# Optimization experiments

Hardware: AMD Instinct MI355X
Metric: run time of the kernel (lower is better)

Reference implementation:

```python
import jax, jax.numpy as jnp
import numpy as np

BN_EPS = 1e-5


def setup_inputs() -> dict:
    key = jax.random.key(0)
    k1, k2, k3 = jax.random.split(key, 3)
    C = 192
    inputs = jax.random.normal(k1, (32, C, 112, 112), dtype=jnp.float32)
    # Depthwise kernels: one 3x3 filter per channel -> OIHW with I=1, groups=C
    w = jax.random.normal(k2, (C, 1, 3, 3), dtype=jnp.float32) * 0.1
    b = jax.random.normal(k3, (C,), dtype=jnp.float32) * 0.1
    gamma = jnp.ones((C,), dtype=jnp.float32)
    beta = jnp.zeros((C,), dtype=jnp.float32)
    return {"inputs": inputs, "w": w, "b": b, "gamma": gamma, "beta": beta}


def reference(inputs, w, b, gamma, beta):
    C = w.shape[0]
    stride = 1
    # Depthwise 3x3 conv (equivalent to the per-channel Conv2d loop + concat)
    y = jax.lax.conv_general_dilated(
        inputs, w,
        window_strides=(stride, stride),
        padding=((1, 1), (1, 1)),
        dimension_numbers=("NCHW", "OIHW", "NCHW"),
        feature_group_count=C,
    ) + b[None, :, None, None]
    # BatchNorm2d in training mode: batch statistics over (N, H, W), biased var
    mean = jnp.mean(y, axis=(0, 2, 3), keepdims=True)
    var = jnp.mean(jnp.square(y - mean), axis=(0, 2, 3), keepdims=True)
    y_hat = (y - mean) * jax.lax.rsqrt(var + BN_EPS)
    z = gamma[None, :, None, None] * y_hat + beta[None, :, None, None]
    # ReLU6
    return jnp.clip(z, 0.0, 6.0)
```

## Files before the change

kernel.cpp:

```cpp
#include <hip/hip_runtime.h>

#define C_   192
#define N_   32
#define H_   112
#define W_   112
#define W4   28
#define V_   4
#define HT   (H_ / V_)
#define P2   (HT * W4)
#define BLK  256
#define GX   ((P2 + BLK - 1) / BLK)

__global__ void zero_acc_kernel(float* __restrict__ acc) {
    for (int i = threadIdx.x; i < 2 * C_; i += blockDim.x) acc[i] = 0.0f;
}

struct Row { float l; float4 m; float r; };

__device__ __forceinline__ Row load_row(const float* __restrict__ row, int j) {
    const float* p = row + 4 * j;
    Row r;
    r.m = *(const float4*)p;
    r.l = (j > 0)      ? p[-1] : 0.0f;
    r.r = (j < W4 - 1) ? p[4]  : 0.0f;
    return r;
}

__device__ __forceinline__ void fma_row(const Row& r, float w0, float w1, float w2,
                                        float4& a) {
    a.x += w0 * r.l   + w1 * r.m.x + w2 * r.m.y;
    a.y += w0 * r.m.x + w1 * r.m.y + w2 * r.m.z;
    a.z += w0 * r.m.y + w1 * r.m.z + w2 * r.m.w;
    a.w += w0 * r.m.z + w1 * r.m.w + w2 * r.r;
}

__device__ __forceinline__ void conv_tile(const float* __restrict__ plane,
                                          int ht, int j, const float* wc,
                                          float4 y[V_]) {
    Row rows[V_ + 2];
    const float* rp = plane + (size_t)(ht * V_) * W_;
    if (ht > 0) rows[0] = load_row(rp - W_, j);
    else        rows[0] = Row{0.f, {0.f, 0.f, 0.f, 0.f}, 0.f};
#pragma unroll
    for (int v = 0; v < V_; ++v) rows[1 + v] = load_row(rp + v * W_, j);
    if (ht < HT - 1) rows[V_ + 1] = load_row(rp + (size_t)V_ * W_, j);
    else             rows[V_ + 1] = Row{0.f, {0.f, 0.f, 0.f, 0.f}, 0.f};

#pragma unroll
    for (int v = 0; v < V_; ++v) {
        float4 a = {0.f, 0.f, 0.f, 0.f};
        fma_row(rows[v],     wc[0], wc[1], wc[2], a);
        fma_row(rows[v + 1], wc[3], wc[4], wc[5], a);
        fma_row(rows[v + 2], wc[6], wc[7], wc[8], a);
        y[v] = a;
    }
}

__global__ __launch_bounds__(BLK) void stats_kernel(const float* __restrict__ in,
                                                    const float* __restrict__ w,
                                                    float* __restrict__ acc) {
    const int nc = blockIdx.y;
    const int c  = nc % C_;
    const int t  = blockIdx.x * BLK + threadIdx.x;

    float wc[9];
#pragma unroll
    for (int k = 0; k < 9; ++k) wc[k] = w[c * 9 + k];

    float s = 0.0f, ss = 0.0f;
    if (t < P2) {
        const int ht = t / W4, j = t % W4;
        const float* plane = in + (size_t)nc * (H_ * W_);
        float4 y[V_];
        conv_tile(plane, ht, j, wc, y);
#pragma unroll
        for (int v = 0; v < V_; ++v) {
            s  += (y[v].x + y[v].y) + (y[v].z + y[v].w);
            ss += (y[v].x * y[v].x + y[v].y * y[v].y)
                + (y[v].z * y[v].z + y[v].w * y[v].w);
        }
    }

#pragma unroll
    for (int off = 32; off > 0; off >>= 1) {
        s  += __shfl_down(s,  off, 64);
        ss += __shfl_down(ss, off, 64);
    }
    __shared__ float ls[BLK / 64], lss[BLK / 64];
    const int lane = threadIdx.x & 63;
    const int wv   = threadIdx.x >> 6;
    if (lane == 0) { ls[wv] = s; lss[wv] = ss; }
    __syncthreads();
    if (threadIdx.x == 0) {
        float S  = 0.f, SS = 0.f;
#pragma unroll
        for (int i = 0; i < BLK / 64; ++i) { S += ls[i]; SS += lss[i]; }
        atomicAdd(&acc[c],      S);
        atomicAdd(&acc[C_ + c], SS);
    }
}

__global__ void finalize_kernel(const float* __restrict__ acc,
                                const float* __restrict__ gamma,
                                const float* __restrict__ beta,
                                float* __restrict__ st) {
    const int c = threadIdx.x;
    if (c < C_) {
        const float M    = (float)N_ * (float)H_ * (float)W_;
        const float mean = acc[c] / M;
        float var        = acc[C_ + c] / M - mean * mean;
        var              = fmaxf(var, 0.0f);
        const float sc   = gamma[c] * rsqrtf(var + 1e-5f);
        st[c]       = sc;
        st[C_ + c]  = beta[c] - sc * mean;
    }
}

__global__ __launch_bounds__(BLK) void apply_kernel(const float* __restrict__ in,
                                                    const float* __restrict__ w,
                                                    const float* __restrict__ st,
                                                    float* __restrict__ out) {
    const int nc = blockIdx.y;
    const int c  = nc % C_;
    const int t  = blockIdx.x * BLK + threadIdx.x;
    if (t >= P2) return;

    float wc[9];
#pragma unroll
    for (int k = 0; k < 9; ++k) wc[k] = w[c * 9 + k];
    const float sc = st[c];
    const float sh = st[C_ + c];

    const int ht = t / W4, j = t % W4;
    const float* plane = in + (size_t)nc * (H_ * W_);
    float4 y[V_];
    conv_tile(plane, ht, j, wc, y);

    float* orow = out + (size_t)nc * (H_ * W_) + (size_t)(ht * V_) * W_ + 4 * j;
#pragma unroll
    for (int v = 0; v < V_; ++v) {
        float4 z;
        z.x = fminf(fmaxf(sc * y[v].x + sh, 0.0f), 6.0f);
        z.y = fminf(fmaxf(sc * y[v].y + sh, 0.0f), 6.0f);
        z.z = fminf(fmaxf(sc * y[v].z + sh, 0.0f), 6.0f);
        z.w = fminf(fmaxf(sc * y[v].w + sh, 0.0f), 6.0f);
        *(float4*)(orow + (size_t)v * W_) = z;
    }
}

extern "C" void kernel_launch(void* const* d_in, const int* in_sizes, int n_in,
                              void* d_out, int out_size, void* d_ws, size_t ws_size,
                              hipStream_t stream) {
    const float* in    = (const float*)d_in[0];
    const float* w     = (const float*)d_in[1];
    const float* gamma = (const float*)d_in[3];
    const float* beta  = (const float*)d_in[4];
    float* out = (float*)d_out;

    float* acc = (float*)d_ws;
    float* st  = acc + 2 * C_;

    hipLaunchKernelGGL(zero_acc_kernel, dim3(1), dim3(64), 0, stream, acc);

    const dim3 grid(GX, N_ * C_);
    hipLaunchKernelGGL(stats_kernel, grid, dim3(BLK), 0, stream, in, w, acc);
    hipLaunchKernelGGL(finalize_kernel, dim3(1), dim3(C_), 0, stream,
                       acc, gamma, beta, st);
    hipLaunchKernelGGL(apply_kernel, grid, dim3(BLK), 0, stream, in, w, st, out);
}
```

Before: 617.2 us.

## Remap threads to 32-lane row tiles with shuffle halos and reversed apply order

Threads are regrouped so each 32-lane half-wave covers one 4-row strip of a plane (28 active lanes), and the grid becomes 1D over all strips. Left and right halo values now come from cross-lane shuffles instead of extra scalar global loads. The stats reduction now does one atomic pair per half-wave, with no shared-memory stage. The apply kernel walks blocks in reverse order so it starts on data the stats pass touched last and is more likely still cached, and it writes output with nontemporal stores. The cost is 4 idle lanes per 32, and many more atomics on the same per-channel accumulators.

```diff
diff --git a/kernel.cpp b/kernel.cpp
--- a/kernel.cpp
+++ b/kernel.cpp
@@ -4,12 +4,15 @@
 #define N_   32
 #define H_   112
 #define W_   112
-#define W4   28
 #define V_   4
 #define HT   (H_ / V_)
-#define P2   (HT * W4)
+#define NC   (N_ * C_)
+#define NRT  (NC * HT)
 #define BLK  256
-#define GX   ((P2 + BLK - 1) / BLK)
+#define HWPB (BLK / 32)
+#define NBLK (NRT / HWPB)
+
+typedef float vf4 __attribute__((ext_vector_type(4)));
 
 __global__ void zero_acc_kernel(float* __restrict__ acc) {
     for (int i = threadIdx.x; i < 2 * C_; i += blockDim.x) acc[i] = 0.0f;
@@ -17,12 +20,14 @@
 
 struct Row { float l; float4 m; float r; };
 
-__device__ __forceinline__ Row load_row(const float* __restrict__ row, int j) {
-    const float* p = row + 4 * j;
+__device__ __forceinline__ Row load_row_sh(const float* __restrict__ p,
+                                           bool has_l, bool has_r) {
     Row r;
     r.m = *(const float4*)p;
-    r.l = (j > 0)      ? p[-1] : 0.0f;
-    r.r = (j < W4 - 1) ? p[4]  : 0.0f;
+    const float lv = __shfl_up(r.m.w, 1, 64);
+    const float rv = __shfl_down(r.m.x, 1, 64);
+    r.l = has_l ? lv : 0.0f;
+    r.r = has_r ? rv : 0.0f;
     return r;
 }
 
@@ -35,17 +40,25 @@
 }
 
 __device__ __forceinline__ void conv_tile(const float* __restrict__ plane,
-                                          int ht, int j, const float* wc,
-                                          float4 y[V_]) {
+                                          int ht, int jeff, bool hl, bool hr,
+                                          const float* wc, float4 y[V_]) {
+    const float* rp = plane + (size_t)(ht * V_) * W_ + 4 * jeff;
     Row rows[V_ + 2];
-    const float* rp = plane + (size_t)(ht * V_) * W_;
-    if (ht > 0) rows[0] = load_row(rp - W_, j);
-    else        rows[0] = Row{0.f, {0.f, 0.f, 0.f, 0.f}, 0.f};
+    {
+        const float* p = (ht > 0) ? (rp - W_) : rp;
+        Row r = load_row_sh(p, hl, hr);
+        if (ht == 0) { r.l = 0.f; r.m = make_float4(0.f, 0.f, 0.f, 0.f); r.r = 0.f; }
+        rows[0] = r;
+    }
 #pragma unroll
-    for (int v = 0; v < V_; ++v) rows[1 + v] = load_row(rp + v * W_, j);
-    if (ht < HT - 1) rows[V_ + 1] = load_row(rp + (size_t)V_ * W_, j);
-    else             rows[V_ + 1] = Row{0.f, {0.f, 0.f, 0.f, 0.f}, 0.f};
-
+    for (int v = 0; v < V_; ++v)
+        rows[1 + v] = load_row_sh(rp + v * W_, hl, hr);
+    {
+        const float* p = (ht < HT - 1) ? (rp + V_ * W_) : rp;
+        Row r = load_row_sh(p, hl, hr);
+        if (ht == HT - 1) { r.l = 0.f; r.m = make_float4(0.f, 0.f, 0.f, 0.f); r.r = 0.f; }
+        rows[V_ + 1] = r;
+    }
 #pragma unroll
     for (int v = 0; v < V_; ++v) {
         float4 a = {0.f, 0.f, 0.f, 0.f};
@@ -56,23 +69,28 @@
     }
 }
 
-__global__ __launch_bounds__(BLK) void stats_kernel(const float* __restrict__ in,
-                                                    const float* __restrict__ w,
-                                                    float* __restrict__ acc) {
-    const int nc = blockIdx.y;
-    const int c  = nc % C_;
-    const int t  = blockIdx.x * BLK + threadIdx.x;
+__global__ __launch_bounds__(BLK, 4) void stats_kernel(const float* __restrict__ in,
+                                                       const float* __restrict__ w,
+                                                       float* __restrict__ acc) {
+    const int tid  = threadIdx.x;
+    const int R    = blockIdx.x * HWPB + (tid >> 5);
+    const int j    = tid & 31;
+    const bool act = (j < 28);
+    const int jeff = act ? j : 27;
+    const int nc   = R / HT;
+    const int ht   = R - nc * HT;
+    const int c    = nc % C_;
 
     float wc[9];
 #pragma unroll
     for (int k = 0; k < 9; ++k) wc[k] = w[c * 9 + k];
 
+    const float* plane = in + (size_t)nc * (H_ * W_);
+    float4 y[V_];
+    conv_tile(plane, ht, jeff, j > 0, j < 27, wc, y);
+
     float s = 0.0f, ss = 0.0f;
-    if (t < P2) {
-        const int ht = t / W4, j = t % W4;
-        const float* plane = in + (size_t)nc * (H_ * W_);
-        float4 y[V_];
-        conv_tile(plane, ht, j, wc, y);
+    if (act) {
 #pragma unroll
         for (int v = 0; v < V_; ++v) {
             s  += (y[v].x + y[v].y) + (y[v].z + y[v].w);
@@ -82,21 +100,13 @@
     }
 
 #pragma unroll
-    for (int off = 32; off > 0; off >>= 1) {
-        s  += __shfl_down(s,  off, 64);
-        ss += __shfl_down(ss, off, 64);
+    for (int off = 16; off > 0; off >>= 1) {
+        s  += __shfl_down(s,  off, 32);
+        ss += __shfl_down(ss, off, 32);
     }
-    __shared__ float ls[BLK / 64], lss[BLK / 64];
-    const int lane = threadIdx.x & 63;
-    const int wv   = threadIdx.x >> 6;
-    if (lane == 0) { ls[wv] = s; lss[wv] = ss; }
-    __syncthreads();
-    if (threadIdx.x == 0) {
-        float S  = 0.f, SS = 0.f;
-#pragma unroll
-        for (int i = 0; i < BLK / 64; ++i) { S += ls[i]; SS += lss[i]; }
-        atomicAdd(&acc[c],      S);
-        atomicAdd(&acc[C_ + c], SS);
+    if (j == 0) {
+        atomicAdd(&acc[c],      s);
+        atomicAdd(&acc[C_ + c], ss);
     }
 }
 
@@ -116,14 +126,19 @@
     }
 }
 
-__global__ __launch_bounds__(BLK) void apply_kernel(const float* __restrict__ in,
-                                                    const float* __restrict__ w,
-                                                    const float* __restrict__ st,
-                                                    float* __restrict__ out) {
-    const int nc = blockIdx.y;
-    const int c  = nc % C_;
-    const int t  = blockIdx.x * BLK + threadIdx.x;
-    if (t >= P2) return;
+__global__ __launch_bounds__(BLK, 4) void apply_kernel(const float* __restrict__ in,
+                                                       const float* __restrict__ w,
+                                                       const float* __restrict__ st,
+                                                       float* __restrict__ out) {
+    const int tid  = threadIdx.x;
+    const int bid  = (int)gridDim.x - 1 - (int)blockIdx.x;
+    const int R    = bid * HWPB + (tid >> 5);
+    const int j    = tid & 31;
+    const bool act = (j < 28);
+    const int jeff = act ? j : 27;
+    const int nc   = R / HT;
+    const int ht   = R - nc * HT;
+    const int c    = nc % C_;
 
     float wc[9];
 #pragma unroll
@@ -131,20 +146,21 @@
     const float sc = st[c];
     const float sh = st[C_ + c];
 
-    const int ht = t / W4, j = t % W4;
     const float* plane = in + (size_t)nc * (H_ * W_);
     float4 y[V_];
-    conv_tile(plane, ht, j, wc, y);
+    conv_tile(plane, ht, jeff, j > 0, j < 27, wc, y);
 
-    float* orow = out + (size_t)nc * (H_ * W_) + (size_t)(ht * V_) * W_ + 4 * j;
+    if (act) {
+        float* orow = out + (size_t)nc * (H_ * W_) + (size_t)(ht * V_) * W_ + 4 * j;
 #pragma unroll
-    for (int v = 0; v < V_; ++v) {
-        float4 z;
-        z.x = fminf(fmaxf(sc * y[v].x + sh, 0.0f), 6.0f);
-        z.y = fminf(fmaxf(sc * y[v].y + sh, 0.0f), 6.0f);
-        z.z = fminf(fmaxf(sc * y[v].z + sh, 0.0f), 6.0f);
-        z.w = fminf(fmaxf(sc * y[v].w + sh, 0.0f), 6.0f);
-        *(float4*)(orow + (size_t)v * W_) = z;
+        for (int v = 0; v < V_; ++v) {
+            float4 z;
+            z.x = fminf(fmaxf(sc * y[v].x + sh, 0.0f), 6.0f);
+            z.y = fminf(fmaxf(sc * y[v].y + sh, 0.0f), 6.0f);
+            z.z = fminf(fmaxf(sc * y[v].z + sh, 0.0f), 6.0f);
+            z.w = fminf(fmaxf(sc * y[v].w + sh, 0.0f), 6.0f);
+            __builtin_nontemporal_store(*(vf4*)&z, (vf4*)(orow + (size_t)v * W_));
+        }
     }
 }
 
@@ -161,10 +177,8 @@
     float* st  = acc + 2 * C_;
 
     hipLaunchKernelGGL(zero_acc_kernel, dim3(1), dim3(64), 0, stream, acc);
-
-    const dim3 grid(GX, N_ * C_);
-    hipLaunchKernelGGL(stats_kernel, grid, dim3(BLK), 0, stream, in, w, acc);
+    hipLaunchKernelGGL(stats_kernel, dim3(NBLK), dim3(BLK), 0, stream, in, w, acc);
     hipLaunchKernelGGL(finalize_kernel, dim3(1), dim3(C_), 0, stream,
                        acc, gamma, beta, st);
-    hipLaunchKernelGGL(apply_kernel, grid, dim3(BLK), 0, stream, in, w, st, out);
+    hipLaunchKernelGGL(apply_kernel, dim3(NBLK), dim3(BLK), 0, stream, in, w, st, out);
 }
```

Measured after the change: 806.1 us. 30.6% more time.
